# Performance work log

Hardware: AMD Instinct MI355X
Metric: run time of the kernel (lower is better)

The kernel has to match this reference:

```python
import jax, jax.numpy as jnp
import numpy as np

B, N, M, Wlen = 4, 20000, 64, 8


def setup_inputs() -> dict:
    key = jax.random.key(0)
    k1, k2, k3, k4 = jax.random.split(key, 4)
    a0 = jax.random.uniform(k1, (B, N), dtype=jnp.float32)
    W = 0.01 * jax.random.normal(k2, (M, M), dtype=jnp.float32)
    X1 = jax.random.randint(k3, (M, N, Wlen, 2), 0, N, dtype=jnp.int64)
    X2 = jax.random.randint(k4, (M, N, Wlen, 2), 0, N, dtype=jnp.int64)
    return {"a0": a0, "W": W, "X1": X1, "X2": X2, "T": 2}


def f_clause_stack(a, X):
    # a: [B,n], X: [m,n,w,2] -> [B,m,n]
    y1 = a[:, X[..., 0]]  # [B,m,n,w] gather
    y2 = a[:, X[..., 1]]
    return jnp.max(y1 * y2, axis=3)


def predicate_forward(a, W, X1, X2, temperature=1.0):
    F1 = f_clause_stack(a, X1)  # [B,m1,n]
    F2 = f_clause_stack(a, X2)  # [B,m2,n]
    pi = jax.nn.softmax((W / temperature).reshape(-1)).reshape(W.shape)  # [m1,m2]
    pi1 = pi.sum(axis=1)  # [m1]
    pi2 = pi.sum(axis=0)  # [m2]
    Eu = jnp.einsum('j,bjn->bn', pi1, F1)
    Ev = jnp.einsum('k,bkn->bn', pi2, F2)
    Mt = jnp.einsum('jk,bkn->bjn', pi, F2)
    Euv = jnp.sum(F1 * Mt, axis=1)
    return Eu + Ev - Euv  # [B,n]


def reference(a0, W, X1, X2, T):
    a = a0
    for _ in range(T):  # T is a small static int
        derived = predicate_forward(a, W, X1, X2)
        # single intensional predicate -> stack/max over predicates is identity
        a = 1.0 - (1.0 - a) * (1.0 - derived)
    return a
```

## Files before the change

kernel.cpp:

```cpp
#include <hip/hip_runtime.h>

#define NN 20000
#define COLS 32

typedef _Float16 f16x2 __attribute__((ext_vector_type(2)));
typedef unsigned short u16x2 __attribute__((ext_vector_type(2)));

union U32H2 { unsigned int u; f16x2 h; };
union U32S2 { unsigned int u; u16x2 s; };

__device__ __forceinline__ f16x2 bc_h2(unsigned int u) { U32H2 x; x.u = u; return x.h; }
__device__ __forceinline__ unsigned int dup_h(float v) {
    _Float16 h = (_Float16)v;
    unsigned short b = __builtin_bit_cast(unsigned short, h);
    return ((unsigned int)b << 16) | b;
}
__device__ __forceinline__ unsigned int pkrtz_u32(float a, float b) {
    return __builtin_bit_cast(unsigned int, __builtin_amdgcn_cvt_pkrtz(a, b));
}

template <int CTRL>
__device__ __forceinline__ unsigned int pkmax_dpp(unsigned int v) {
    unsigned int d = (unsigned int)__builtin_amdgcn_update_dpp(
        0, (int)v, CTRL, 0xF, 0xF, true);
    U32S2 a, b; a.u = v; b.u = d;
    a.s = __builtin_elementwise_max(a.s, b.s);
    return a.u;
}
__device__ __forceinline__ unsigned int octmax_u16x2(unsigned int v) {
    v = pkmax_dpp<0xB1>(v);
    v = pkmax_dpp<0x4E>(v);
    v = pkmax_dpp<0x141>(v);
    return v;
}

__global__ __launch_bounds__(1024) void prep_kernel(const float* __restrict__ W,
                                                    unsigned int* __restrict__ pi_pk,
                                                    unsigned int* __restrict__ pi_t_pk,
                                                    unsigned int* __restrict__ pi1_pk,
                                                    unsigned int* __restrict__ pi2_pk) {
    __shared__ float red[1024];
    __shared__ float piL[4096];
    int t = threadIdx.x;
    float4 wv = ((const float4*)W)[t];
    float m = fmaxf(fmaxf(wv.x, wv.y), fmaxf(wv.z, wv.w));
    red[t] = m; __syncthreads();
    for (int s = 512; s > 0; s >>= 1) {
        if (t < s) red[t] = fmaxf(red[t], red[t + s]);
        __syncthreads();
    }
    m = red[0];
    __syncthreads();
    float e0 = expf(wv.x - m), e1 = expf(wv.y - m);
    float e2 = expf(wv.z - m), e3 = expf(wv.w - m);
    red[t] = e0 + e1 + e2 + e3;
    __syncthreads();
    for (int s = 512; s > 0; s >>= 1) {
        if (t < s) red[t] += red[t + s];
        __syncthreads();
    }
    float inv = 1.0f / red[0];
    float p[4] = { e0 * inv, e1 * inv, e2 * inv, e3 * inv };
#pragma unroll
    for (int i = 0; i < 4; i++) {
        int f = t * 4 + i;
        piL[f] = p[i];
        unsigned int d = dup_h(p[i]);
        pi_pk[f] = d;
        pi_t_pk[(f & 63) * 64 + (f >> 6)] = d;
    }
    __syncthreads();
    if (t < 64) {
        float s = 0.f;
        for (int k = 0; k < 64; k++) s += piL[t * 64 + k];
        pi1_pk[t] = dup_h(s);
    } else if (t < 128) {
        int k = t - 64;
        float s = 0.f;
        for (int j = 0; j < 64; j++) s += piL[j * 64 + k];
        pi2_pk[k] = dup_h(s);
    }
}

__global__ __launch_bounds__(1024) void pack_kernel(const float* __restrict__ a0,
                                                    unsigned int* __restrict__ T0) {
    int i = blockIdx.x * 1024 + threadIdx.x;
    if (i < NN) {
        unsigned int b0 = __float2uint_rn(__saturatef(a0[i]) * 255.0f);
        unsigned int b1 = __float2uint_rn(__saturatef(a0[NN + i]) * 255.0f);
        unsigned int b2 = __float2uint_rn(__saturatef(a0[2 * NN + i]) * 255.0f);
        unsigned int b3 = __float2uint_rn(__saturatef(a0[3 * NN + i]) * 255.0f);
        T0[i] = b0 | (b1 << 8) | (b2 << 16) | (b3 << 24);
    }
}

__device__ __forceinline__ void phase1(
    const unsigned int* __restrict__ tab,
    unsigned int (* __restrict__ Ftb)[COLS][2],
    const int* __restrict__ X1, const int* __restrict__ X2,
    int nb, int cn, int widu, int ni, int w) {
    const float sc = 1.0f / 65025.0f;
    int loff[4];
#pragma unroll
    for (int oc = 0; oc < 4; ++oc) {
        int n = nb + oc * 8 + ni;
        int nc = n < NN ? n : NN - 1;
        loff[oc] = nc * 64 + w * 8;
    }
    int2 q5[4];
    {
        const int row = widu, k = row & 63;
        const char* Xb = (const char*)((row >> 6) ? X2 : X1) + (unsigned)(k * NN) * 64u;
#pragma unroll
        for (int oc = 0; oc < 4; ++oc) q5[oc] = *(const int2*)(Xb + loff[oc]);
    }
#pragma unroll
    for (int rr = 0; rr < 8; ++rr) {
        int2 qn[4];
        if (rr < 7) {
            const int row = widu + 16 * (rr + 1), k = row & 63;
            const char* Xb = (const char*)((row >> 6) ? X2 : X1) + (unsigned)(k * NN) * 64u;
#pragma unroll
            for (int oc = 0; oc < 4; ++oc) qn[oc] = *(const int2*)(Xb + loff[oc]);
        }
        const int row = widu + 16 * rr;
        unsigned int ga[4], gb[4];
#pragma unroll
        for (int oc = 0; oc < 4; ++oc) { ga[oc] = tab[q5[oc].x]; gb[oc] = tab[q5[oc].y]; }
#pragma unroll
        for (int oc = 0; oc < 4; ++oc) {
            unsigned int ea = ga[oc] & 0x00FF00FFu;
            unsigned int oa = (ga[oc] >> 8) & 0x00FF00FFu;
            unsigned int eb = gb[oc] & 0x00FF00FFu;
            unsigned int ob = (gb[oc] >> 8) & 0x00FF00FFu;
            U32S2 pe, po, xb;
            pe.u = ea; xb.u = eb; pe.s = pe.s * xb.s;
            po.u = oa; xb.u = ob; po.s = po.s * xb.s;
            unsigned int peu = octmax_u16x2(pe.u);
            unsigned int pou = octmax_u16x2(po.u);
            int col = oc * 8 + ni;
            if (w == 0 && col < cn) {
                float f0 = (float)(peu & 0xFFFFu) * sc;
                float f1 = (float)(pou & 0xFFFFu) * sc;
                float f2 = (float)(peu >> 16) * sc;
                float f3 = (float)(pou >> 16) * sc;
                *(uint2*)&Ftb[row][col][0] =
                    make_uint2(pkrtz_u32(f0, f1), pkrtz_u32(f2, f3));
            }
        }
#pragma unroll
        for (int oc = 0; oc < 4; ++oc) q5[oc] = qn[oc];
    }
}

__device__ __forceinline__ float2 phase2(
    const unsigned int (* __restrict__ Ftb)[COLS][2],
    const unsigned int* __restrict__ pi_t_pk,
    const unsigned int* __restrict__ pi1_pk,
    const unsigned int* __restrict__ pi2_pk,
    int qu, int bp, int n_l) {
    f16x2 zero = {(_Float16)0, (_Float16)0};
    f16x2 f1v[8];
    f16x2 eu = zero;
#pragma unroll
    for (int jj = 0; jj < 8; ++jj) {
        f1v[jj] = bc_h2(Ftb[qu * 8 + jj][n_l][bp]);
        eu += bc_h2(pi1_pk[qu * 8 + jj]) * f1v[jj];
    }
    f16x2 euv = zero, ev = zero;
#pragma unroll 8
    for (int k = 0; k < 64; ++k) {
        f16x2 f2 = bc_h2(Ftb[64 + k][n_l][bp]);
        const uint4* pt = (const uint4*)(pi_t_pk + k * 64 + qu * 8);
        uint4 w0 = pt[0], w1 = pt[1];
        f16x2 ts = bc_h2(w0.x) * f1v[0] + bc_h2(w0.y) * f1v[1] +
                   bc_h2(w0.z) * f1v[2] + bc_h2(w0.w) * f1v[3] +
                   bc_h2(w1.x) * f1v[4] + bc_h2(w1.y) * f1v[5] +
                   bc_h2(w1.z) * f1v[6] + bc_h2(w1.w) * f1v[7];
        euv += f2 * ts;
        if (qu == 0) ev += bc_h2(pi2_pk[k]) * f2;
    }
    float p0 = (float)eu[0] - (float)euv[0];
    float p1 = (float)eu[1] - (float)euv[1];
    if (qu == 0) { p0 += (float)ev[0]; p1 += (float)ev[1]; }
    return make_float2(p0, p1);
}

template <int ITER>
__global__ __launch_bounds__(1024, 4) void fused_iter(
    const unsigned int* __restrict__ Tsrc,
    const int* __restrict__ X1, const int* __restrict__ X2,
    const unsigned int* __restrict__ pi_t_pk,
    const unsigned int* __restrict__ pi1_pk,
    const unsigned int* __restrict__ pi2_pk,
    const float* __restrict__ a0,
    unsigned int* __restrict__ Tdst, float* __restrict__ outP) {
    __shared__ unsigned int tab[NN];
    __shared__ unsigned int Ft[2][128][COLS][2];
    __shared__ float redp[2][8][COLS][4];

    const int t = threadIdx.x;
    for (int i = t; i < NN; i += 1024) tab[i] = Tsrc[i];

    const int bid = (int)blockIdx.x;
    const int bstart = bid < 32 ? bid * 79 : 32 * 79 + (bid - 32) * 78;
    const int bcnt = bid < 32 ? 79 : 78;
    const int nbs[3] = { bstart, bstart + 32, bstart + 64 };
    const int cns[3] = { 32, 32, bcnt - 64 };

    const int wid = t >> 6, lane = t & 63, ni = lane >> 3, w = lane & 7;
    const int q = t >> 7, bp = (t >> 6) & 1, n_l = t & 63;
    const int widu = __builtin_amdgcn_readfirstlane(wid);
    const int qu = __builtin_amdgcn_readfirstlane(q);

    __syncthreads();
    phase1(tab, Ft[0], X1, X2, nbs[0], cns[0], widu, ni, w);
    __syncthreads();

    for (int c = 0; c < 3; ++c) {
        const int cur = c & 1;
        if (n_l < cns[c]) {
            float2 pp = phase2(Ft[cur], pi_t_pk, pi1_pk, pi2_pk, qu, bp, n_l);
            *(float2*)&redp[cur][q][n_l][bp * 2] = pp;
        }
        if (c < 2)
            phase1(tab, Ft[cur ^ 1], X1, X2, nbs[c + 1], cns[c + 1], widu, ni, w);
        __syncthreads();
        if (t < cns[c]) {
            int gn = nbs[c] + t;
            float d0 = 0.f, d1 = 0.f, d2 = 0.f, d3 = 0.f;
#pragma unroll
            for (int q8 = 0; q8 < 8; ++q8) {
                d0 += redp[cur][q8][t][0];
                d1 += redp[cur][q8][t][1];
                d2 += redp[cur][q8][t][2];
                d3 += redp[cur][q8][t][3];
            }
            float ap0, ap1, ap2, ap3;
            if (ITER == 1) {
                ap0 = a0[gn]; ap1 = a0[NN + gn];
                ap2 = a0[2 * NN + gn]; ap3 = a0[3 * NN + gn];
            } else {
                unsigned int tv = tab[gn];
                ap0 = (float)(tv & 255u) * (1.0f / 255.0f);
                ap1 = (float)((tv >> 8) & 255u) * (1.0f / 255.0f);
                ap2 = (float)((tv >> 16) & 255u) * (1.0f / 255.0f);
                ap3 = (float)(tv >> 24) * (1.0f / 255.0f);
            }
            float an0 = 1.0f - (1.0f - ap0) * (1.0f - d0);
            float an1 = 1.0f - (1.0f - ap1) * (1.0f - d1);
            float an2 = 1.0f - (1.0f - ap2) * (1.0f - d2);
            float an3 = 1.0f - (1.0f - ap3) * (1.0f - d3);
            if (ITER == 1) {
                unsigned int b0 = __float2uint_rn(__saturatef(an0) * 255.0f);
                unsigned int b1 = __float2uint_rn(__saturatef(an1) * 255.0f);
                unsigned int b2 = __float2uint_rn(__saturatef(an2) * 255.0f);
                unsigned int b3 = __float2uint_rn(__saturatef(an3) * 255.0f);
                Tdst[gn] = b0 | (b1 << 8) | (b2 << 16) | (b3 << 24);
            } else {
                outP[gn] = an0;
                outP[NN + gn] = an1;
                outP[2 * NN + gn] = an2;
                outP[3 * NN + gn] = an3;
            }
        }
    }
}

extern "C" void kernel_launch(void* const* d_in, const int* in_sizes, int n_in,
                              void* d_out, int out_size, void* d_ws, size_t ws_size,
                              hipStream_t stream) {
    const float* a0 = (const float*)d_in[0];
    const float* W = (const float*)d_in[1];
    const int* X1 = (const int*)d_in[2];
    const int* X2 = (const int*)d_in[3];
    float* out = (float*)d_out;

    if (ws_size < (size_t)193280) return;
    unsigned int* pi_pk  = (unsigned int*)d_ws;
    unsigned int* pi_t   = (unsigned int*)((char*)d_ws + 16384);
    unsigned int* pi1_pk = (unsigned int*)((char*)d_ws + 32768);
    unsigned int* pi2_pk = (unsigned int*)((char*)d_ws + 33024);
    unsigned int* T0     = (unsigned int*)((char*)d_ws + 33280);
    unsigned int* T1     = (unsigned int*)((char*)d_ws + 113280);

    prep_kernel<<<1, 1024, 0, stream>>>(W, pi_pk, pi_t, pi1_pk, pi2_pk);
    pack_kernel<<<20, 1024, 0, stream>>>(a0, T0);
    fused_iter<1><<<256, 1024, 0, stream>>>(T0, X1, X2, pi_t, pi1_pk, pi2_pk,
                                            a0, T1, nullptr);
    fused_iter<2><<<256, 1024, 0, stream>>>(T1, X1, X2, pi_t, pi1_pk, pi2_pk,
                                            nullptr, nullptr, out);
}
```

Baseline: 258.2 us.

## Process two 40-column chunks per block with transposed padded F-tile layout

Each block now handles its columns in two chunks of up to 40 instead of three chunks of up to 32. The phase1/phase2 software overlap through a double-buffered F tile is replaced by a single padded [row][pair][41] buffer, with a barrier between the two phases. Phase1 now prefetches index loads two rows ahead and handles five column groups per lane. Fewer chunks and barriers and more gather work in flight per wave are the aim, but the cross-phase overlap is lost, and there is register pressure from the deeper prefetch and some idle lanes in phase2 (40 of 64 used).

```diff
diff --git a/kernel.cpp b/kernel.cpp
--- a/kernel.cpp
+++ b/kernel.cpp
@@ -1,7 +1,8 @@
 #include <hip/hip_runtime.h>
 
 #define NN 20000
-#define COLS 32
+#define COLS 40
+#define CPAD 41
 
 typedef _Float16 f16x2 __attribute__((ext_vector_type(2)));
 typedef unsigned short u16x2 __attribute__((ext_vector_type(2)));
@@ -96,39 +97,44 @@
 
 __device__ __forceinline__ void phase1(
     const unsigned int* __restrict__ tab,
-    unsigned int (* __restrict__ Ftb)[COLS][2],
+    unsigned int (* __restrict__ Ftb)[2][CPAD],
     const int* __restrict__ X1, const int* __restrict__ X2,
     int nb, int cn, int widu, int ni, int w) {
     const float sc = 1.0f / 65025.0f;
-    int loff[4];
-#pragma unroll
-    for (int oc = 0; oc < 4; ++oc) {
+    int loff[5];
+#pragma unroll
+    for (int oc = 0; oc < 5; ++oc) {
         int n = nb + oc * 8 + ni;
         int nc = n < NN ? n : NN - 1;
         loff[oc] = nc * 64 + w * 8;
     }
-    int2 q5[4];
-    {
-        const int row = widu, k = row & 63;
+    int2 qb[2][5];
+#pragma unroll
+    for (int d = 0; d < 2; ++d) {
+        const int row = widu + 16 * d, k = row & 63;
         const char* Xb = (const char*)((row >> 6) ? X2 : X1) + (unsigned)(k * NN) * 64u;
 #pragma unroll
-        for (int oc = 0; oc < 4; ++oc) q5[oc] = *(const int2*)(Xb + loff[oc]);
+        for (int oc = 0; oc < 5; ++oc) qb[d][oc] = *(const int2*)(Xb + loff[oc]);
     }
 #pragma unroll
     for (int rr = 0; rr < 8; ++rr) {
-        int2 qn[4];
-        if (rr < 7) {
-            const int row = widu + 16 * (rr + 1), k = row & 63;
-            const char* Xb = (const char*)((row >> 6) ? X2 : X1) + (unsigned)(k * NN) * 64u;
-#pragma unroll
-            for (int oc = 0; oc < 4; ++oc) qn[oc] = *(const int2*)(Xb + loff[oc]);
+        const int cur = rr & 1;
+        unsigned int ga[5], gb[5];
+#pragma unroll
+        for (int oc = 0; oc < 5; ++oc) {
+            ga[oc] = tab[qb[cur][oc].x];
+            gb[oc] = tab[qb[cur][oc].y];
+        }
+        if (rr < 6) {
+            const int row2 = widu + 16 * (rr + 2), k2 = row2 & 63;
+            const char* Xb = (const char*)((row2 >> 6) ? X2 : X1)
+                           + (unsigned)(k2 * NN) * 64u;
+#pragma unroll
+            for (int oc = 0; oc < 5; ++oc) qb[cur][oc] = *(const int2*)(Xb + loff[oc]);
         }
         const int row = widu + 16 * rr;
-        unsigned int ga[4], gb[4];
-#pragma unroll
-        for (int oc = 0; oc < 4; ++oc) { ga[oc] = tab[q5[oc].x]; gb[oc] = tab[q5[oc].y]; }
-#pragma unroll
-        for (int oc = 0; oc < 4; ++oc) {
+#pragma unroll
+        for (int oc = 0; oc < 5; ++oc) {
             unsigned int ea = ga[oc] & 0x00FF00FFu;
             unsigned int oa = (ga[oc] >> 8) & 0x00FF00FFu;
             unsigned int eb = gb[oc] & 0x00FF00FFu;
@@ -144,17 +150,15 @@
                 float f1 = (float)(pou & 0xFFFFu) * sc;
                 float f2 = (float)(peu >> 16) * sc;
                 float f3 = (float)(pou >> 16) * sc;
-                *(uint2*)&Ftb[row][col][0] =
-                    make_uint2(pkrtz_u32(f0, f1), pkrtz_u32(f2, f3));
-            }
-        }
-#pragma unroll
-        for (int oc = 0; oc < 4; ++oc) q5[oc] = qn[oc];
+                Ftb[row][0][col] = pkrtz_u32(f0, f1);
+                Ftb[row][1][col] = pkrtz_u32(f2, f3);
+            }
+        }
     }
 }
 
 __device__ __forceinline__ float2 phase2(
-    const unsigned int (* __restrict__ Ftb)[COLS][2],
+    const unsigned int (* __restrict__ Ftb)[2][CPAD],
     const unsigned int* __restrict__ pi_t_pk,
     const unsigned int* __restrict__ pi1_pk,
     const unsigned int* __restrict__ pi2_pk,
@@ -164,13 +168,13 @@
     f16x2 eu = zero;
 #pragma unroll
     for (int jj = 0; jj < 8; ++jj) {
-        f1v[jj] = bc_h2(Ftb[qu * 8 + jj][n_l][bp]);
+        f1v[jj] = bc_h2(Ftb[qu * 8 + jj][bp][n_l]);
         eu += bc_h2(pi1_pk[qu * 8 + jj]) * f1v[jj];
     }
     f16x2 euv = zero, ev = zero;
 #pragma unroll 8
     for (int k = 0; k < 64; ++k) {
-        f16x2 f2 = bc_h2(Ftb[64 + k][n_l][bp]);
+        f16x2 f2 = bc_h2(Ftb[64 + k][bp][n_l]);
         const uint4* pt = (const uint4*)(pi_t_pk + k * 64 + qu * 8);
         uint4 w0 = pt[0], w1 = pt[1];
         f16x2 ts = bc_h2(w0.x) * f1v[0] + bc_h2(w0.y) * f1v[1] +
@@ -196,8 +200,8 @@
     const float* __restrict__ a0,
     unsigned int* __restrict__ Tdst, float* __restrict__ outP) {
     __shared__ unsigned int tab[NN];
-    __shared__ unsigned int Ft[2][128][COLS][2];
-    __shared__ float redp[2][8][COLS][4];
+    __shared__ unsigned int Ft[128][2][CPAD];
+    __shared__ float redp[8][64][4];
 
     const int t = threadIdx.x;
     for (int i = t; i < NN; i += 1024) tab[i] = Tsrc[i];
@@ -205,8 +209,7 @@
     const int bid = (int)blockIdx.x;
     const int bstart = bid < 32 ? bid * 79 : 32 * 79 + (bid - 32) * 78;
     const int bcnt = bid < 32 ? 79 : 78;
-    const int nbs[3] = { bstart, bstart + 32, bstart + 64 };
-    const int cns[3] = { 32, 32, bcnt - 64 };
+    const int c0 = (bcnt + 1) >> 1;
 
     const int wid = t >> 6, lane = t & 63, ni = lane >> 3, w = lane & 7;
     const int q = t >> 7, bp = (t >> 6) & 1, n_l = t & 63;
@@ -214,27 +217,29 @@
     const int qu = __builtin_amdgcn_readfirstlane(q);
 
     __syncthreads();
-    phase1(tab, Ft[0], X1, X2, nbs[0], cns[0], widu, ni, w);
-    __syncthreads();
-
-    for (int c = 0; c < 3; ++c) {
-        const int cur = c & 1;
-        if (n_l < cns[c]) {
-            float2 pp = phase2(Ft[cur], pi_t_pk, pi1_pk, pi2_pk, qu, bp, n_l);
-            *(float2*)&redp[cur][q][n_l][bp * 2] = pp;
-        }
-        if (c < 2)
-            phase1(tab, Ft[cur ^ 1], X1, X2, nbs[c + 1], cns[c + 1], widu, ni, w);
-        __syncthreads();
-        if (t < cns[c]) {
-            int gn = nbs[c] + t;
+
+    for (int ch = 0; ch < 2; ++ch) {
+        const int nb = bstart + (ch ? c0 : 0);
+        const int cn = ch ? (bcnt - c0) : c0;
+
+        phase1(tab, Ft, X1, X2, nb, cn, widu, ni, w);
+        __syncthreads();
+
+        if (n_l < cn) {
+            float2 pp = phase2(Ft, pi_t_pk, pi1_pk, pi2_pk, qu, bp, n_l);
+            *(float2*)&redp[q][n_l][bp * 2] = pp;
+        }
+        __syncthreads();
+
+        if (t < cn) {
+            int gn = nb + t;
             float d0 = 0.f, d1 = 0.f, d2 = 0.f, d3 = 0.f;
 #pragma unroll
             for (int q8 = 0; q8 < 8; ++q8) {
-                d0 += redp[cur][q8][t][0];
-                d1 += redp[cur][q8][t][1];
-                d2 += redp[cur][q8][t][2];
-                d3 += redp[cur][q8][t][3];
+                d0 += redp[q8][t][0];
+                d1 += redp[q8][t][1];
+                d2 += redp[q8][t][2];
+                d3 += redp[q8][t][3];
             }
             float ap0, ap1, ap2, ap3;
             if (ITER == 1) {
```

Measured after the change: 250.0 us. 1.03x faster.
